# Kernel tuning notes

Measured on AMD Instinct MI355X. Metric: run time of the kernel, lower is better.

Reference implementation:

```python
import jax, jax.numpy as jnp
import numpy as np

N_NODES = 50000
N_EDGES = 600000
N_GRAPHS = 2000
IN_FEATS = 64
HIDDEN = 128


def setup_inputs() -> dict:
    key = jax.random.key(0)
    ks = jax.random.split(key, 16)
    d = {}
    d["feats_node"] = jax.random.normal(ks[0], (N_NODES, IN_FEATS), jnp.float32)
    d["feats_graph"] = jax.random.normal(ks[1], (N_GRAPHS, 3), jnp.float32)
    s = 0.05
    d["W1"] = jax.random.normal(ks[2], (IN_FEATS, HIDDEN), jnp.float32) * s
    d["b1"] = jnp.zeros((HIDDEN,), jnp.float32)
    d["W2"] = jax.random.normal(ks[3], (HIDDEN, HIDDEN), jnp.float32) * s
    d["b2"] = jnp.zeros((HIDDEN,), jnp.float32)
    d["W3"] = jax.random.normal(ks[4], (HIDDEN, HIDDEN), jnp.float32) * s
    d["b3"] = jnp.zeros((HIDDEN,), jnp.float32)
    d["Wl1"] = jax.random.normal(ks[5], (HIDDEN + 3, 2 * HIDDEN), jnp.float32) * s
    d["bl1"] = jnp.zeros((2 * HIDDEN,), jnp.float32)
    d["Wl2"] = jax.random.normal(ks[6], (2 * HIDDEN, 2 * HIDDEN), jnp.float32) * s
    d["bl2"] = jnp.zeros((2 * HIDDEN,), jnp.float32)
    d["Wl3"] = jax.random.normal(ks[7], (2 * HIDDEN, 1), jnp.float32) * s
    d["bl3"] = jnp.zeros((1,), jnp.float32)
    d["src"] = jax.random.randint(ks[8], (N_EDGES,), 0, N_NODES, jnp.int32)
    d["dst"] = jax.random.randint(ks[9], (N_EDGES,), 0, N_NODES, jnp.int32)
    d["graph_ids"] = jnp.sort(jax.random.randint(ks[10], (N_NODES,), 0, N_GRAPHS, jnp.int32))
    return d


def reference(feats_node, feats_graph, W1, b1, W2, b2, W3, b3,
              Wl1, bl1, Wl2, bl2, Wl3, bl3, src, dst, graph_ids):
    N = feats_node.shape[0]
    ones_e = jnp.ones((src.shape[0],), feats_node.dtype)
    # DGL GraphConv norm='both': symmetric degree normalization, degrees clamped to >=1
    deg_out = jax.ops.segment_sum(ones_e, src, num_segments=N)
    deg_in = jax.ops.segment_sum(ones_e, dst, num_segments=N)
    c_out = jax.lax.rsqrt(jnp.maximum(deg_out, 1.0))[:, None]  # [N,1]
    c_in = jax.lax.rsqrt(jnp.maximum(deg_in, 1.0))[:, None]

    def gconv(x, W, b):
        h = x * c_out                                   # scale by src out-degree
        agg = jax.ops.segment_sum(h[src], dst, num_segments=N)  # gather + scatter-add
        return (agg * c_in) @ W + b

    x = jax.nn.relu(gconv(feats_node, W1, b1))
    x = jax.nn.relu(gconv(x, W2, b2))
    y_nodes = gconv(x, W3, b3)                          # [N, HIDDEN]

    # readout_nodes op='mean' over batched graphs
    G = feats_graph.shape[0]
    sum_y = jax.ops.segment_sum(y_nodes, graph_ids, num_segments=G)
    cnt = jax.ops.segment_sum(jnp.ones((N,), y_nodes.dtype), graph_ids, num_segments=G)
    mean_y = sum_y / jnp.maximum(cnt, 1.0)[:, None]     # [G, HIDDEN]

    y = jnp.concatenate([mean_y, feats_graph], axis=1)  # [G, HIDDEN+3]
    y = jax.nn.relu(y @ Wl1 + bl1)
    y = jax.nn.relu(y @ Wl2 + bl2)
    return (y @ Wl3 + bl3).reshape(-1)                  # [G]
```

## Files before the change

### kernel.cpp

```cpp
#include <hip/hip_runtime.h>

constexpr int NNODES = 50000;
constexpr int NEDGES = 600000;
constexpr int NGRAPH = 2000;
constexpr int F0     = 64;
constexpr int H      = 128;
constexpr int H2     = 256;
constexpr int NB     = 49;

static __device__ __forceinline__ void fma4(float4& acc, float s, const float4& w) {
    acc.x = fmaf(s, w.x, acc.x);
    acc.y = fmaf(s, w.y, acc.y);
    acc.z = fmaf(s, w.z, acc.z);
    acc.w = fmaf(s, w.w, acc.w);
}

__global__ void k_deg(const int* __restrict__ src, const int* __restrict__ dst,
                      int* __restrict__ dout, int* __restrict__ din) {
    int t = blockIdx.x * 256 + threadIdx.x;
    if (t * 4 >= NEDGES) return;
    int4 s4 = ((const int4*)src)[t];
    int4 d4 = ((const int4*)dst)[t];
    atomicAdd(&dout[s4.x], 1);
    atomicAdd(&dout[s4.y], 1);
    atomicAdd(&dout[s4.z], 1);
    atomicAdd(&dout[s4.w], 1);
    atomicAdd(&din[d4.x], 1);
    atomicAdd(&din[d4.y], 1);
    atomicAdd(&din[d4.z], 1);
    atomicAdd(&din[d4.w], 1);
}

__global__ __launch_bounds__(1024) void k_scan1(const int* __restrict__ deg,
                                                int* __restrict__ row_start,
                                                int* __restrict__ partials,
                                                float* __restrict__ c_in) {
    __shared__ int wsum[16];
    int idx  = blockIdx.x * 1024 + threadIdx.x;
    int lane = threadIdx.x & 63;
    int wid  = threadIdx.x >> 6;
    int v = (idx < NNODES) ? deg[idx] : 0;
    if (idx < NNODES) c_in[idx] = rsqrtf(fmaxf((float)v, 1.0f));
    int incl = v;
#pragma unroll
    for (int off = 1; off < 64; off <<= 1) {
        int t = __shfl_up(incl, off);
        if (lane >= off) incl += t;
    }
    if (lane == 63) wsum[wid] = incl;
    __syncthreads();
    if (wid == 0) {
        int w = (lane < 16) ? wsum[lane] : 0;
        int wincl = w;
#pragma unroll
        for (int off = 1; off < 16; off <<= 1) {
            int t = __shfl_up(wincl, off);
            if (lane >= off) wincl += t;
        }
        if (lane < 16) wsum[lane] = wincl - w;
    }
    __syncthreads();
    int excl = wsum[wid] + incl - v;
    if (idx < NNODES) row_start[idx] = excl;
    if (threadIdx.x == 1023) partials[blockIdx.x] = excl + v;
}

__global__ void k_scan2(int* __restrict__ partials) {
    int lane = threadIdx.x;
    int v = (lane < NB) ? partials[lane] : 0;
    int incl = v;
#pragma unroll
    for (int off = 1; off < 64; off <<= 1) {
        int t = __shfl_up(incl, off);
        if (lane >= off) incl += t;
    }
    if (lane < NB) partials[lane] = incl - v;
    if (lane == NB - 1) partials[NB] = incl;
}

__global__ __launch_bounds__(1024) void k_scan3(int* __restrict__ row_start,
                                                const int* __restrict__ partials,
                                                const int* __restrict__ dout,
                                                float* __restrict__ c_out,
                                                int* __restrict__ cursor) {
    int idx = blockIdx.x * 1024 + threadIdx.x;
    if (idx < NNODES) {
        row_start[idx] += partials[blockIdx.x];
        c_out[idx] = rsqrtf(fmaxf((float)dout[idx], 1.0f));
        cursor[idx] = 0;
    } else if (idx == NNODES) {
        row_start[NNODES] = partials[NB];
    }
}

__global__ void k_fill(const int* __restrict__ src, const int* __restrict__ dst,
                       const int* __restrict__ row_start, int* __restrict__ cursor,
                       int* __restrict__ csr_src) {
    int t = blockIdx.x * 256 + threadIdx.x;
    if (t * 4 >= NEDGES) return;
    int4 s4 = ((const int4*)src)[t];
    int4 d4 = ((const int4*)dst)[t];
    int p;
    p = atomicAdd(&cursor[d4.x], 1); csr_src[row_start[d4.x] + p] = s4.x;
    p = atomicAdd(&cursor[d4.y], 1); csr_src[row_start[d4.y] + p] = s4.y;
    p = atomicAdd(&cursor[d4.z], 1); csr_src[row_start[d4.z] + p] = s4.z;
    p = atomicAdd(&cursor[d4.w], 1); csr_src[row_start[d4.w] + p] = s4.w;
}

__global__ void k_gbounds(const int* __restrict__ gids, int* __restrict__ gstart) {
    int n = blockIdx.x * 256 + threadIdx.x;
    if (n > NNODES) return;
    if (n == 0) {
        int g0 = gids[0];
        for (int g = 0; g <= g0; ++g) gstart[g] = 0;
    } else if (n == NNODES) {
        int gl = gids[NNODES - 1];
        for (int g = gl + 1; g <= NGRAPH; ++g) gstart[g] = NNODES;
    } else {
        int a = gids[n - 1], b = gids[n];
        for (int g = a + 1; g <= b; ++g) gstart[g] = n;
    }
}

template <int F>
static __device__ __forceinline__ void gather_body(const float* __restrict__ x,
                                                   const float* __restrict__ c_out,
                                                   const int* __restrict__ row_start,
                                                   const int* __restrict__ csr_src,
                                                   float* __restrict__ agg) {
    int wid  = (blockIdx.x * 256 + threadIdx.x) >> 6;
    int lane = threadIdx.x & 63;
    if (wid >= NNODES) return;
    int beg = row_start[wid], end = row_start[wid + 1];
    if (F == 128) {
        const float2* x2 = (const float2*)x;
        float2 acc = make_float2(0.f, 0.f);
#pragma unroll 4
        for (int i = beg; i < end; ++i) {
            int s = csr_src[i];
            float co = c_out[s];
            float2 v = x2[(long)s * 64 + lane];
            acc.x += v.x * co;
            acc.y += v.y * co;
        }
        ((float2*)agg)[(long)wid * 64 + lane] = acc;
    } else {
        float acc = 0.f;
#pragma unroll 4
        for (int i = beg; i < end; ++i) {
            int s = csr_src[i];
            acc += x[(long)s * F + lane] * c_out[s];
        }
        agg[(long)wid * F + lane] = acc;
    }
}

__global__ __launch_bounds__(256) void k_gather1(const float* __restrict__ x,
                                                 const float* __restrict__ c_out,
                                                 const int* __restrict__ row_start,
                                                 const int* __restrict__ csr_src,
                                                 float* __restrict__ agg) {
    gather_body<F0>(x, c_out, row_start, csr_src, agg);
}
__global__ __launch_bounds__(256) void k_gather2(const float* __restrict__ x,
                                                 const float* __restrict__ c_out,
                                                 const int* __restrict__ row_start,
                                                 const int* __restrict__ csr_src,
                                                 float* __restrict__ agg) {
    gather_body<H>(x, c_out, row_start, csr_src, agg);
}
__global__ __launch_bounds__(256) void k_gather3(const float* __restrict__ x,
                                                 const float* __restrict__ c_out,
                                                 const int* __restrict__ row_start,
                                                 const int* __restrict__ csr_src,
                                                 float* __restrict__ agg) {
    gather_body<H>(x, c_out, row_start, csr_src, agg);
}

template <int K, bool RELU>
static __device__ __forceinline__ void gemm_body(const float* __restrict__ A,
                                                 const float* __restrict__ c_in,
                                                 const float* __restrict__ W,
                                                 const float* __restrict__ b,
                                                 float* __restrict__ out) {
    __shared__ float sW[K * H];
    for (int i = threadIdx.x; i < K * (H / 4); i += 512)
        ((float4*)sW)[i] = ((const float4*)W)[i];
    __syncthreads();

    const int c = threadIdx.x & 31;
    const int r = threadIdx.x >> 5;
    const long base = (long)blockIdx.x * 128 + r * 8;

    float4 acc[8];
#pragma unroll
    for (int i = 0; i < 8; ++i) acc[i] = make_float4(0.f, 0.f, 0.f, 0.f);

    const float4* Ap = (const float4*)A + base * (K / 4);

    for (int k4 = 0; k4 < K / 4; ++k4) {
        const float4 w0 = *(const float4*)&sW[(4 * k4 + 0) * H + 4 * c];
        const float4 w1 = *(const float4*)&sW[(4 * k4 + 1) * H + 4 * c];
        const float4 w2 = *(const float4*)&sW[(4 * k4 + 2) * H + 4 * c];
        const float4 w3 = *(const float4*)&sW[(4 * k4 + 3) * H + 4 * c];
#pragma unroll
        for (int i = 0; i < 8; ++i) {
            float4 a = Ap[(long)i * (K / 4) + k4];
            fma4(acc[i], a.x, w0);
            fma4(acc[i], a.y, w1);
            fma4(acc[i], a.z, w2);
            fma4(acc[i], a.w, w3);
        }
    }

    const float4 bv = ((const float4*)b)[c];
#pragma unroll
    for (int i = 0; i < 8; ++i) {
        long n = base + i;
        if (n < NNODES) {
            float ci = c_in[n];
            float4 res;
            res.x = fmaf(acc[i].x, ci, bv.x);
            res.y = fmaf(acc[i].y, ci, bv.y);
            res.z = fmaf(acc[i].z, ci, bv.z);
            res.w = fmaf(acc[i].w, ci, bv.w);
            if (RELU) {
                res.x = fmaxf(res.x, 0.f);
                res.y = fmaxf(res.y, 0.f);
                res.z = fmaxf(res.z, 0.f);
                res.w = fmaxf(res.w, 0.f);
            }
            ((float4*)out)[n * (H / 4) + c] = res;
        }
    }
}

__global__ __launch_bounds__(512) void k_gemm1(const float* __restrict__ A,
                                               const float* __restrict__ c_in,
                                               const float* __restrict__ W,
                                               const float* __restrict__ b,
                                               float* __restrict__ out) {
    gemm_body<F0, true>(A, c_in, W, b, out);
}
__global__ __launch_bounds__(512) void k_gemm2(const float* __restrict__ A,
                                               const float* __restrict__ c_in,
                                               const float* __restrict__ W,
                                               const float* __restrict__ b,
                                               float* __restrict__ out) {
    gemm_body<H, true>(A, c_in, W, b, out);
}
__global__ __launch_bounds__(512) void k_gemm3(const float* __restrict__ A,
                                               const float* __restrict__ c_in,
                                               const float* __restrict__ W,
                                               const float* __restrict__ b,
                                               float* __restrict__ out) {
    gemm_body<H, false>(A, c_in, W, b, out);
}

__global__ __launch_bounds__(256) void k_head(const float* __restrict__ y,
                                              const int* __restrict__ gstart,
                                              const float* __restrict__ fg,
                                              const float* __restrict__ Wl1,
                                              const float* __restrict__ bl1,
                                              const float* __restrict__ Wl2,
                                              const float* __restrict__ bl2,
                                              const float* __restrict__ Wl3,
                                              const float* __restrict__ bl3,
                                              float* __restrict__ out) {
    __shared__ float smean[4][H];
    __shared__ float sh1[4][H2];
    __shared__ float sh2[4][H2];

    const int w    = threadIdx.x >> 6;
    const int lane = threadIdx.x & 63;
    const int g    = blockIdx.x * 4 + w;

    {
        int beg = gstart[g], end = gstart[g + 1];
        const float2* y2 = (const float2*)y;
        float2 acc = make_float2(0.f, 0.f);
        for (int n = beg; n < end; ++n) {
            float2 v = y2[(long)n * 64 + lane];
            acc.x += v.x;
            acc.y += v.y;
        }
        float inv = 1.0f / fmaxf((float)(end - beg), 1.0f);
        ((float2*)smean[w])[lane] = make_float2(acc.x * inv, acc.y * inv);
    }

    {
        float4 acc = ((const float4*)bl1)[lane];
        for (int k = 0; k < H; ++k)
            fma4(acc, smean[w][k], ((const float4*)(Wl1 + (long)k * H2))[lane]);
#pragma unroll
        for (int k = 0; k < 3; ++k)
            fma4(acc, fg[g * 3 + k], ((const float4*)(Wl1 + (long)(H + k) * H2))[lane]);
        acc.x = fmaxf(acc.x, 0.f); acc.y = fmaxf(acc.y, 0.f);
        acc.z = fmaxf(acc.z, 0.f); acc.w = fmaxf(acc.w, 0.f);
        ((float4*)sh1[w])[lane] = acc;
    }

    {
        float4 acc = ((const float4*)bl2)[lane];
        for (int k = 0; k < H2; ++k)
            fma4(acc, sh1[w][k], ((const float4*)(Wl2 + (long)k * H2))[lane]);
        acc.x = fmaxf(acc.x, 0.f); acc.y = fmaxf(acc.y, 0.f);
        acc.z = fmaxf(acc.z, 0.f); acc.w = fmaxf(acc.w, 0.f);
        ((float4*)sh2[w])[lane] = acc;
    }

    {
        float sum = sh2[w][lane] * Wl3[lane]
                  + sh2[w][lane + 64] * Wl3[lane + 64]
                  + sh2[w][lane + 128] * Wl3[lane + 128]
                  + sh2[w][lane + 192] * Wl3[lane + 192];
        for (int off = 32; off; off >>= 1)
            sum += __shfl_down(sum, off);
        if (lane == 0) out[g] = sum + bl3[0];
    }
}

extern "C" void kernel_launch(void* const* d_in, const int* in_sizes, int n_in,
                              void* d_out, int out_size, void* d_ws, size_t ws_size,
                              hipStream_t stream) {
    const float* feats_node  = (const float*)d_in[0];
    const float* feats_graph = (const float*)d_in[1];
    const float* W1 = (const float*)d_in[2];
    const float* b1 = (const float*)d_in[3];
    const float* W2 = (const float*)d_in[4];
    const float* b2 = (const float*)d_in[5];
    const float* W3 = (const float*)d_in[6];
    const float* b3 = (const float*)d_in[7];
    const float* Wl1 = (const float*)d_in[8];
    const float* bl1 = (const float*)d_in[9];
    const float* Wl2 = (const float*)d_in[10];
    const float* bl2 = (const float*)d_in[11];
    const float* Wl3 = (const float*)d_in[12];
    const float* bl3 = (const float*)d_in[13];
    const int* src  = (const int*)d_in[14];
    const int* dst  = (const int*)d_in[15];
    const int* gids = (const int*)d_in[16];
    float* out = (float*)d_out;

    float* ws = (float*)d_ws;
    float* c_out     = ws;
    float* c_in      = c_out + 50048;
    float* A         = c_in + 50048;
    float* B         = A + (size_t)NNODES * H;
    int*   row_start = (int*)(B + (size_t)NNODES * H);
    int*   csr_src   = row_start + 50176;
    int*   cursor    = csr_src + NEDGES;
    int*   gstart    = cursor + 50176;
    int*   partials  = gstart + 2048;
    int*   dout      = partials + 64;
    int*   din       = dout + 50048;

    hipMemsetAsync(dout, 0, 2 * 50048 * sizeof(int), stream);
    k_deg<<<(NEDGES / 4 + 255) / 256, 256, 0, stream>>>(src, dst, dout, din);

    k_scan1<<<NB, 1024, 0, stream>>>(din, row_start, partials, c_in);
    k_scan2<<<1, 64, 0, stream>>>(partials);
    k_scan3<<<NB, 1024, 0, stream>>>(row_start, partials, dout, c_out, cursor);
    k_fill<<<(NEDGES / 4 + 255) / 256, 256, 0, stream>>>(src, dst, row_start, cursor, csr_src);
    k_gbounds<<<(NNODES + 256) / 256, 256, 0, stream>>>(gids, gstart);

    const int GEMM_GRID = (NNODES + 127) / 128;

    k_gather1<<<NNODES / 4, 256, 0, stream>>>(feats_node, c_out, row_start, csr_src, A);
    k_gemm1<<<GEMM_GRID, 512, 0, stream>>>(A, c_in, W1, b1, B);

    k_gather2<<<NNODES / 4, 256, 0, stream>>>(B, c_out, row_start, csr_src, A);
    k_gemm2<<<GEMM_GRID, 512, 0, stream>>>(A, c_in, W2, b2, B);

    k_gather3<<<NNODES / 4, 256, 0, stream>>>(B, c_out, row_start, csr_src, A);
    k_gemm3<<<GEMM_GRID, 512, 0, stream>>>(A, c_in, W3, b3, B);

    k_head<<<NGRAPH / 4, 256, 0, stream>>>(B, gstart, feats_graph,
                                           Wl1, bl1, Wl2, bl2, Wl3, bl3, out);
}
```

Baseline: 428.6 us.

## Record edge ranks during degree count, fuse scan/bounds kernels, fold c_out into GEMM

The degree kernel now keeps the atomicAdd return value as each edge's rank within its destination. CSR fill then scatters with no second pass of atomics and no cursor array. The partial-sum scan is folded into k_scan3, and the graph-boundary computation is merged into the same kernel, removing two launches. The c_out scaling moves from the gather inner loops into the epilogue of GEMM1 and GEMM2, so layers 2 and 3 skip the per-edge c_out load. The head kernel processes 8 graphs per 512-thread block. Rank is stored in buffer A before A is reused, which relies on ordering on the stream.

```diff
diff --git a/kernel.cpp b/kernel.cpp
--- a/kernel.cpp
+++ b/kernel.cpp
@@ -16,19 +16,22 @@
 }
 
 __global__ void k_deg(const int* __restrict__ src, const int* __restrict__ dst,
-                      int* __restrict__ dout, int* __restrict__ din) {
+                      int* __restrict__ dout, int* __restrict__ din,
+                      int* __restrict__ rank) {
     int t = blockIdx.x * 256 + threadIdx.x;
     if (t * 4 >= NEDGES) return;
     int4 s4 = ((const int4*)src)[t];
     int4 d4 = ((const int4*)dst)[t];
+    int4 r4;
+    r4.x = atomicAdd(&din[d4.x], 1);
+    r4.y = atomicAdd(&din[d4.y], 1);
+    r4.z = atomicAdd(&din[d4.z], 1);
+    r4.w = atomicAdd(&din[d4.w], 1);
+    ((int4*)rank)[t] = r4;
     atomicAdd(&dout[s4.x], 1);
     atomicAdd(&dout[s4.y], 1);
     atomicAdd(&dout[s4.z], 1);
     atomicAdd(&dout[s4.w], 1);
-    atomicAdd(&din[d4.x], 1);
-    atomicAdd(&din[d4.y], 1);
-    atomicAdd(&din[d4.z], 1);
-    atomicAdd(&din[d4.w], 1);
 }
 
 __global__ __launch_bounds__(1024) void k_scan1(const int* __restrict__ deg,
@@ -65,94 +68,57 @@
     if (threadIdx.x == 1023) partials[blockIdx.x] = excl + v;
 }
 
-__global__ void k_scan2(int* __restrict__ partials) {
-    int lane = threadIdx.x;
-    int v = (lane < NB) ? partials[lane] : 0;
-    int incl = v;
-#pragma unroll
-    for (int off = 1; off < 64; off <<= 1) {
-        int t = __shfl_up(incl, off);
-        if (lane >= off) incl += t;
-    }
-    if (lane < NB) partials[lane] = incl - v;
-    if (lane == NB - 1) partials[NB] = incl;
-}
-
 __global__ __launch_bounds__(1024) void k_scan3(int* __restrict__ row_start,
                                                 const int* __restrict__ partials,
                                                 const int* __restrict__ dout,
                                                 float* __restrict__ c_out,
-                                                int* __restrict__ cursor) {
+                                                const int* __restrict__ gids,
+                                                int* __restrict__ gstart) {
+    __shared__ int soff[2];
+    if (threadIdx.x < 64) {
+        int lane = threadIdx.x;
+        int v = (lane < NB) ? partials[lane] : 0;
+        int incl = v;
+#pragma unroll
+        for (int off = 1; off < 64; off <<= 1) {
+            int t = __shfl_up(incl, off);
+            if (lane >= off) incl += t;
+        }
+        if (lane == (int)blockIdx.x) soff[0] = incl - v;
+        if (lane == NB - 1) soff[1] = incl;
+    }
+    __syncthreads();
     int idx = blockIdx.x * 1024 + threadIdx.x;
     if (idx < NNODES) {
-        row_start[idx] += partials[blockIdx.x];
+        row_start[idx] += soff[0];
         c_out[idx] = rsqrtf(fmaxf((float)dout[idx], 1.0f));
-        cursor[idx] = 0;
     } else if (idx == NNODES) {
-        row_start[NNODES] = partials[NB];
+        row_start[NNODES] = soff[1];
+    }
+    if (idx == 0) {
+        int g0 = gids[0];
+        for (int g = 0; g <= g0; ++g) gstart[g] = 0;
+    } else if (idx == NNODES) {
+        int gl = gids[NNODES - 1];
+        for (int g = gl + 1; g <= NGRAPH; ++g) gstart[g] = NNODES;
+    } else if (idx < NNODES) {
+        int a = gids[idx - 1], b = gids[idx];
+        for (int g = a + 1; g <= b; ++g) gstart[g] = idx;
     }
 }
 
 __global__ void k_fill(const int* __restrict__ src, const int* __restrict__ dst,
-                       const int* __restrict__ row_start, int* __restrict__ cursor,
+                       const int* __restrict__ row_start, const int* __restrict__ rank,
                        int* __restrict__ csr_src) {
     int t = blockIdx.x * 256 + threadIdx.x;
     if (t * 4 >= NEDGES) return;
     int4 s4 = ((const int4*)src)[t];
     int4 d4 = ((const int4*)dst)[t];
-    int p;
-    p = atomicAdd(&cursor[d4.x], 1); csr_src[row_start[d4.x] + p] = s4.x;
-    p = atomicAdd(&cursor[d4.y], 1); csr_src[row_start[d4.y] + p] = s4.y;
-    p = atomicAdd(&cursor[d4.z], 1); csr_src[row_start[d4.z] + p] = s4.z;
-    p = atomicAdd(&cursor[d4.w], 1); csr_src[row_start[d4.w] + p] = s4.w;
-}
-
-__global__ void k_gbounds(const int* __restrict__ gids, int* __restrict__ gstart) {
-    int n = blockIdx.x * 256 + threadIdx.x;
-    if (n > NNODES) return;
-    if (n == 0) {
-        int g0 = gids[0];
-        for (int g = 0; g <= g0; ++g) gstart[g] = 0;
-    } else if (n == NNODES) {
-        int gl = gids[NNODES - 1];
-        for (int g = gl + 1; g <= NGRAPH; ++g) gstart[g] = NNODES;
-    } else {
-        int a = gids[n - 1], b = gids[n];
-        for (int g = a + 1; g <= b; ++g) gstart[g] = n;
-    }
-}
-
-template <int F>
-static __device__ __forceinline__ void gather_body(const float* __restrict__ x,
-                                                   const float* __restrict__ c_out,
-                                                   const int* __restrict__ row_start,
-                                                   const int* __restrict__ csr_src,
-                                                   float* __restrict__ agg) {
-    int wid  = (blockIdx.x * 256 + threadIdx.x) >> 6;
-    int lane = threadIdx.x & 63;
-    if (wid >= NNODES) return;
-    int beg = row_start[wid], end = row_start[wid + 1];
-    if (F == 128) {
-        const float2* x2 = (const float2*)x;
-        float2 acc = make_float2(0.f, 0.f);
-#pragma unroll 4
-        for (int i = beg; i < end; ++i) {
-            int s = csr_src[i];
-            float co = c_out[s];
-            float2 v = x2[(long)s * 64 + lane];
-            acc.x += v.x * co;
-            acc.y += v.y * co;
-        }
-        ((float2*)agg)[(long)wid * 64 + lane] = acc;
-    } else {
-        float acc = 0.f;
-#pragma unroll 4
-        for (int i = beg; i < end; ++i) {
-            int s = csr_src[i];
-            acc += x[(long)s * F + lane] * c_out[s];
-        }
-        agg[(long)wid * F + lane] = acc;
-    }
+    int4 r4 = ((const int4*)rank)[t];
+    csr_src[row_start[d4.x] + r4.x] = s4.x;
+    csr_src[row_start[d4.y] + r4.y] = s4.y;
+    csr_src[row_start[d4.z] + r4.z] = s4.z;
+    csr_src[row_start[d4.w] + r4.w] = s4.w;
 }
 
 __global__ __launch_bounds__(256) void k_gather1(const float* __restrict__ x,
@@ -160,26 +126,56 @@
                                                  const int* __restrict__ row_start,
                                                  const int* __restrict__ csr_src,
                                                  float* __restrict__ agg) {
-    gather_body<F0>(x, c_out, row_start, csr_src, agg);
-}
+    int wid  = (blockIdx.x * 256 + threadIdx.x) >> 6;
+    int lane = threadIdx.x & 63;
+    if (wid >= NNODES) return;
+    int beg = row_start[wid], end = row_start[wid + 1];
+    float acc = 0.f;
+#pragma unroll 4
+    for (int i = beg; i < end; ++i) {
+        int s = csr_src[i];
+        acc += x[(long)s * F0 + lane] * c_out[s];
+    }
+    agg[(long)wid * F0 + lane] = acc;
+}
+
+static __device__ __forceinline__ void gather_h_body(const float* __restrict__ x,
+                                                     const int* __restrict__ row_start,
+                                                     const int* __restrict__ csr_src,
+                                                     float* __restrict__ agg) {
+    int wid  = (blockIdx.x * 256 + threadIdx.x) >> 6;
+    int lane = threadIdx.x & 63;
+    if (wid >= NNODES) return;
+    int beg = row_start[wid], end = row_start[wid + 1];
+    const float2* x2 = (const float2*)x;
+    float2 acc = make_float2(0.f, 0.f);
+#pragma unroll 4
+    for (int i = beg; i < end; ++i) {
+        int s = csr_src[i];
+        float2 v = x2[(long)s * 64 + lane];
+        acc.x += v.x;
+        acc.y += v.y;
+    }
+    ((float2*)agg)[(long)wid * 64 + lane] = acc;
+}
+
 __global__ __launch_bounds__(256) void k_gather2(const float* __restrict__ x,
-                                                 const float* __restrict__ c_out,
                                                  const int* __restrict__ row_start,
                                                  const int* __restrict__ csr_src,
                                                  float* __restrict__ agg) {
-    gather_body<H>(x, c_out, row_start, csr_src, agg);
+    gather_h_body(x, row_start, csr_src, agg);
 }
 __global__ __launch_bounds__(256) void k_gather3(const float* __restrict__ x,
-                                                 const float* __restrict__ c_out,
                                                  const int* __restrict__ row_start,
                                                  const int* __restrict__ csr_src,
                                                  float* __restrict__ agg) {
-    gather_body<H>(x, c_out, row_start, csr_src, agg);
-}
-
-template <int K, bool RELU>
+    gather_h_body(x, row_start, csr_src, agg);
+}
+
+template <int K, bool RELU, bool COSCALE>
 static __device__ __forceinline__ void gemm_body(const float* __restrict__ A,
                                                  const float* __restrict__ c_in,
+                                                 const float* __restrict__ c_out,
                                                  const float* __restrict__ W,
                                                  const float* __restrict__ b,
                                                  float* __restrict__ out) {
@@ -230,6 +226,10 @@
                 res.z = fmaxf(res.z, 0.f);
                 res.w = fmaxf(res.w, 0.f);
             }
+            if (COSCALE) {
+                float co = c_out[n];
+                res.x *= co; res.y *= co; res.z *= co; res.w *= co;
+            }
             ((float4*)out)[n * (H / 4) + c] = res;
         }
     }
@@ -237,27 +237,30 @@
 
 __global__ __launch_bounds__(512) void k_gemm1(const float* __restrict__ A,
                                                const float* __restrict__ c_in,
+                                               const float* __restrict__ c_out,
                                                const float* __restrict__ W,
                                                const float* __restrict__ b,
                                                float* __restrict__ out) {
-    gemm_body<F0, true>(A, c_in, W, b, out);
+    gemm_body<F0, true, true>(A, c_in, c_out, W, b, out);
 }
 __global__ __launch_bounds__(512) void k_gemm2(const float* __restrict__ A,
                                                const float* __restrict__ c_in,
+                                               const float* __restrict__ c_out,
                                                const float* __restrict__ W,
                                                const float* __restrict__ b,
                                                float* __restrict__ out) {
-    gemm_body<H, true>(A, c_in, W, b, out);
+    gemm_body<H, true, true>(A, c_in, c_out, W, b, out);
 }
 __global__ __launch_bounds__(512) void k_gemm3(const float* __restrict__ A,
                                                const float* __restrict__ c_in,
+                                               const float* __restrict__ c_out,
                                                const float* __restrict__ W,
                                                const float* __restrict__ b,
                                                float* __restrict__ out) {
-    gemm_body<H, false>(A, c_in, W, b, out);
-}
-
-__global__ __launch_bounds__(256) void k_head(const float* __restrict__ y,
+    gemm_body<H, false, false>(A, c_in, c_out, W, b, out);
+}
+
+__global__ __launch_bounds__(512) void k_head(const float* __restrict__ y,
                                               const int* __restrict__ gstart,
                                               const float* __restrict__ fg,
                                               const float* __restrict__ Wl1,
@@ -267,13 +270,13 @@
                                               const float* __restrict__ Wl3,
                                               const float* __restrict__ bl3,
                                               float* __restrict__ out) {
-    __shared__ float smean[4][H];
-    __shared__ float sh1[4][H2];
-    __shared__ float sh2[4][H2];
+    __shared__ float smean[8][H];
+    __shared__ float sh1[8][H2];
+    __shared__ float sh2[8][H2];
 
     const int w    = threadIdx.x >> 6;
     const int lane = threadIdx.x & 63;
-    const int g    = blockIdx.x * 4 + w;
+    const int g    = blockIdx.x * 8 + w;
 
     {
         int beg = gstart[g], end = gstart[g + 1];
@@ -349,32 +352,30 @@
     float* B         = A + (size_t)NNODES * H;
     int*   row_start = (int*)(B + (size_t)NNODES * H);
     int*   csr_src   = row_start + 50176;
-    int*   cursor    = csr_src + NEDGES;
-    int*   gstart    = cursor + 50176;
+    int*   gstart    = csr_src + NEDGES;
     int*   partials  = gstart + 2048;
     int*   dout      = partials + 64;
     int*   din       = dout + 50048;
+    int*   rank      = (int*)A;
 
     hipMemsetAsync(dout, 0, 2 * 50048 * sizeof(int), stream);
-    k_deg<<<(NEDGES / 4 + 255) / 256, 256, 0, stream>>>(src, dst, dout, din);
+    k_deg<<<(NEDGES / 4 + 255) / 256, 256, 0, stream>>>(src, dst, dout, din, rank);
 
     k_scan1<<<NB, 1024, 0, stream>>>(din, row_start, partials, c_in);
-    k_scan2<<<1, 64, 0, stream>>>(partials);
-    k_scan3<<<NB, 1024, 0, stream>>>(row_start, partials, dout, c_out, cursor);
-    k_fill<<<(NEDGES / 4 + 255) / 256, 256, 0, stream>>>(src, dst, row_start, cursor, csr_src);
-    k_gbounds<<<(NNODES + 256) / 256, 256, 0, stream>>>(gids, gstart);
+    k_scan3<<<NB, 1024, 0, stream>>>(row_start, partials, dout, c_out, gids, gstart);
+    k_fill<<<(NEDGES / 4 + 255) / 256, 256, 0, stream>>>(src, dst, row_start, rank, csr_src);
 
     const int GEMM_GRID = (NNODES + 127) / 128;
 
     k_gather1<<<NNODES / 4, 256, 0, stream>>>(feats_node, c_out, row_start, csr_src, A);
-    k_gemm1<<<GEMM_GRID, 512, 0, stream>>>(A, c_in, W1, b1, B);
-
-    k_gather2<<<NNODES / 4, 256, 0, stream>>>(B, c_out, row_start, csr_src, A);
-    k_gemm2<<<GEMM_GRID, 512, 0, stream>>>(A, c_in, W2, b2, B);
-
-    k_gather3<<<NNODES / 4, 256, 0, stream>>>(B, c_out, row_start, csr_src, A);
-    k_gemm3<<<GEMM_GRID, 512, 0, stream>>>(A, c_in, W3, b3, B);
-
-    k_head<<<NGRAPH / 4, 256, 0, stream>>>(B, gstart, feats_graph,
+    k_gemm1<<<GEMM_GRID, 512, 0, stream>>>(A, c_in, c_out, W1, b1, B);
+
+    k_gather2<<<NNODES / 4, 256, 0, stream>>>(B, row_start, csr_src, A);
+    k_gemm2<<<GEMM_GRID, 512, 0, stream>>>(A, c_in, c_out, W2, b2, B);
+
+    k_gather3<<<NNODES / 4, 256, 0, stream>>>(B, row_start, csr_src, A);
+    k_gemm3<<<GEMM_GRID, 512, 0, stream>>>(A, c_in, c_out, W3, b3, B);
+
+    k_head<<<NGRAPH / 8, 512, 0, stream>>>(B, gstart, feats_graph,
                                            Wl1, bl1, Wl2, bl2, Wl3, bl3, out);
 }
```

Result: faster. 407.1 us (-5.0%).
